# Kernel tuning notes

Measured on AMD Instinct MI355X. Metric: run time of the kernel, lower is better.

## Reference

```python
import jax, jax.numpy as jnp
import numpy as np

D_MODEL = 1024


def setup_inputs() -> dict:
    key = jax.random.key(0)
    ks = jax.random.split(key, 9)
    d = D_MODEL
    s = 1.0 / np.sqrt(d)
    return {
        "x": jax.random.normal(ks[0], (4, 2048, d), dtype=jnp.float32),
        "w_q": jax.random.normal(ks[1], (d, d), dtype=jnp.float32) * s,
        "b_q": jnp.zeros((d,), dtype=jnp.float32),
        "w_k": jax.random.normal(ks[2], (d, d), dtype=jnp.float32) * s,
        "b_k": jnp.zeros((d,), dtype=jnp.float32),
        "w_v": jax.random.normal(ks[3], (d, d), dtype=jnp.float32) * s,
        "b_v": jnp.zeros((d,), dtype=jnp.float32),
        "w_out": jax.random.normal(ks[4], (d, d), dtype=jnp.float32) * s,
        "b_out": jnp.zeros((d,), dtype=jnp.float32),
    }


def reference(x, w_q, b_q, w_k, b_k, w_v, b_v, w_out, b_out):
    d_model = x.shape[-1]
    # torch Linear: y = x @ W^T + b
    Q = jnp.einsum("bsd,ed->bse", x, w_q) + b_q
    K = jnp.einsum("bsd,ed->bse", x, w_k) + b_k
    V = jnp.einsum("bsd,ed->bse", x, w_v) + b_v
    scores = jnp.einsum("bqd,bkd->bqk", Q, K) / jnp.sqrt(jnp.float32(d_model)).astype(x.dtype)
    attn = jax.nn.softmax(scores, axis=-1)
    out = jnp.einsum("bqk,bkd->bqd", attn, V)
    return jnp.einsum("bsd,ed->bse", out, w_out) + b_out
```

## Files before the change

### kernel.cpp

```cpp
#include <hip/hip_runtime.h>


typedef __bf16 bf16x8 __attribute__((ext_vector_type(8)));
typedef float f32x4 __attribute__((ext_vector_type(4)));
typedef unsigned short ushort8 __attribute__((ext_vector_type(8)));

__device__ __forceinline__ unsigned short f32_to_bf16(float f) {
  unsigned int u = __float_as_uint(f);
  u += 0x7fffu + ((u >> 16) & 1u);
  return (unsigned short)(u >> 16);
}

__device__ __forceinline__ float bf16_to_f32(unsigned short u) {
  return __uint_as_float((unsigned int)u << 16);
}

__device__ __forceinline__ void load_lds16(const void* g, void* l) {
  __builtin_amdgcn_global_load_lds(
      (const __attribute__((address_space(1))) void*)g,
      (__attribute__((address_space(3))) void*)l, 16, 0, 0);
}

__global__ __launch_bounds__(256) void cast_f32_bf16(
    const float4* __restrict__ in, ushort4* __restrict__ out, int n4) {
  int i = blockIdx.x * 256 + threadIdx.x;
  if (i < n4) {
    float4 f = in[i];
    ushort4 u;
    u.x = f32_to_bf16(f.x);
    u.y = f32_to_bf16(f.y);
    u.z = f32_to_bf16(f.z);
    u.w = f32_to_bf16(f.w);
    out[i] = u;
  }
}

__global__ __launch_bounds__(256) void cast_weights(
    const float4* __restrict__ wq, const float4* __restrict__ wk,
    const float4* __restrict__ wv, const float4* __restrict__ wo,
    ushort4* __restrict__ wqkb, ushort4* __restrict__ wvb,
    ushort4* __restrict__ wob) {
  const int b = blockIdx.x;
  const int seg = b >> 10;
  const int idx = ((b & 1023) << 8) + threadIdx.x;
  const float4* src = seg == 0 ? wq : seg == 1 ? wk : seg == 2 ? wv : wo;
  ushort4* dst = seg == 0 ? wqkb
               : seg == 1 ? (wqkb + 262144)
               : seg == 2 ? wvb : wob;
  float4 f = src[idx];
  ushort4 u;
  u.x = f32_to_bf16(f.x);
  u.y = f32_to_bf16(f.y);
  u.z = f32_to_bf16(f.z);
  u.w = f32_to_bf16(f.w);
  dst[idx] = u;
}

__global__ __launch_bounds__(256) void concat_bias(
    const float* __restrict__ bq, const float* __restrict__ bk,
    float* __restrict__ bqk) {
  int i = blockIdx.x * 256 + threadIdx.x;
  bqk[i] = (i < 1024) ? bq[i] : bk[i - 1024];
}

__global__ __launch_bounds__(256) void gemm_bt(
    const unsigned short* __restrict__ A, const unsigned short* __restrict__ B,
    void* __restrict__ C, const float* __restrict__ bias,
    int M, int N, int K, int ldA, int ldB, int ldC,
    float alpha, int out_bf16, int bias_mode,
    long long sA, long long sB, long long sC) {
  __shared__ unsigned short As[128 * 64];
  __shared__ unsigned short Bs[128 * 64];

  const int bz = blockIdx.z;
  A += (long long)bz * sA;
  B += (long long)bz * sB;

  const int bm = blockIdx.y, bn = blockIdx.x;
  const int tid = threadIdx.x;
  const int lane = tid & 63, wave = tid >> 6;
  const int wr = wave >> 1, wc = wave & 1;
  const int l16 = lane & 15, quad = lane >> 4;

  f32x4 acc[4][4] = {};

  const int srow = tid >> 3;
  const int xr = srow & 7;
  const int scol = ((tid & 7) ^ xr) * 8;
  const unsigned short* gA = A + (long long)(bm * 128 + srow) * ldA + scol;
  const unsigned short* gB = B + (long long)(bn * 128 + srow) * ldB + scol;
  char* ldsA = (char*)As + wave * 1024;
  char* ldsB = (char*)Bs + wave * 1024;

  for (int k0 = 0; k0 < K; k0 += 64) {
#pragma unroll
    for (int r = 0; r < 4; r++)
      load_lds16(gA + k0 + (long long)r * 32 * ldA, ldsA + r * 4096);
#pragma unroll
    for (int r = 0; r < 4; r++)
      load_lds16(gB + k0 + (long long)r * 32 * ldB, ldsB + r * 4096);
    __syncthreads();

    const int swz = l16 & 7;
#pragma unroll
    for (int kk = 0; kk < 64; kk += 32) {
      bf16x8 af[4], bf[4];
      const int lc = (kk >> 3) + quad;
      const int pco = (lc ^ swz) * 8;
#pragma unroll
      for (int mi = 0; mi < 4; mi++)
        af[mi] = *(const bf16x8*)(As + (wr * 64 + mi * 16 + l16) * 64 + pco);
#pragma unroll
      for (int ni = 0; ni < 4; ni++)
        bf[ni] = *(const bf16x8*)(Bs + (wc * 64 + ni * 16 + l16) * 64 + pco);
#pragma unroll
      for (int mi = 0; mi < 4; mi++)
#pragma unroll
        for (int ni = 0; ni < 4; ni++)
          acc[mi][ni] = __builtin_amdgcn_mfma_f32_16x16x32_bf16(
              af[mi], bf[ni], acc[mi][ni], 0, 0, 0);
    }
    __syncthreads();
  }

  const int orow0 = bm * 128 + wr * 64 + quad * 4;
  const int ocol0 = bn * 128 + wc * 64 + l16;
  if (out_bf16) {
    unsigned short* Cp = (unsigned short*)C + (long long)bz * sC;
#pragma unroll
    for (int mi = 0; mi < 4; mi++)
#pragma unroll
      for (int ni = 0; ni < 4; ni++) {
        const int col = ocol0 + ni * 16;
        const float cb = (bias_mode == 1) ? bias[col] : 0.f;
#pragma unroll
        for (int r = 0; r < 4; r++) {
          const int row = orow0 + mi * 16 + r;
          const float bv = (bias_mode == 2) ? bias[row] : cb;
          const float o = acc[mi][ni][r] * alpha + bv;
          Cp[(long long)row * ldC + col] = f32_to_bf16(o);
        }
      }
  } else {
    float* Cp = (float*)C + (long long)bz * sC;
#pragma unroll
    for (int mi = 0; mi < 4; mi++)
#pragma unroll
      for (int ni = 0; ni < 4; ni++) {
        const int col = ocol0 + ni * 16;
        const float cb = (bias_mode == 1) ? bias[col] : 0.f;
#pragma unroll
        for (int r = 0; r < 4; r++) {
          const int row = orow0 + mi * 16 + r;
          const float bv = (bias_mode == 2) ? bias[row] : cb;
          const float o = acc[mi][ni][r] * alpha + bv;
          Cp[(long long)row * ldC + col] = o;
        }
      }
  }
}

__global__ __launch_bounds__(256) void softmax_rows_bf16(
    unsigned short* __restrict__ S) {
  const long long row = blockIdx.x;
  unsigned short* s = S + row * 2048;
  const int t = threadIdx.x;
  ushort8 u = *(const ushort8*)(s + t * 8);
  float v[8];
  float mx = -3.4e38f;
#pragma unroll
  for (int i = 0; i < 8; i++) {
    v[i] = bf16_to_f32(u[i]);
    mx = fmaxf(mx, v[i]);
  }
#pragma unroll
  for (int o = 32; o >= 1; o >>= 1) mx = fmaxf(mx, __shfl_xor(mx, o));
  __shared__ float red[4], red2[4];
  if ((t & 63) == 0) red[t >> 6] = mx;
  __syncthreads();
  mx = fmaxf(fmaxf(red[0], red[1]), fmaxf(red[2], red[3]));
  float sum = 0.f;
#pragma unroll
  for (int i = 0; i < 8; i++) {
    v[i] = __expf(v[i] - mx);
    sum += v[i];
  }
#pragma unroll
  for (int o = 32; o >= 1; o >>= 1) sum += __shfl_xor(sum, o);
  if ((t & 63) == 0) red2[t >> 6] = sum;
  __syncthreads();
  sum = red2[0] + red2[1] + red2[2] + red2[3];
  const float inv = 1.0f / sum;
  ushort8 w;
#pragma unroll
  for (int i = 0; i < 8; i++) w[i] = f32_to_bf16(v[i] * inv);
  *(ushort8*)(s + t * 8) = w;
}

extern "C" void kernel_launch(void* const* d_in, const int* in_sizes, int n_in,
                              void* d_out, int out_size, void* d_ws,
                              size_t ws_size, hipStream_t stream) {
  const float* x = (const float*)d_in[0];
  const float* wq = (const float*)d_in[1];
  const float* bq = (const float*)d_in[2];
  const float* wk = (const float*)d_in[3];
  const float* bk = (const float*)d_in[4];
  const float* wv = (const float*)d_in[5];
  const float* bv = (const float*)d_in[6];
  const float* wo = (const float*)d_in[7];
  const float* bo = (const float*)d_in[8];
  float* out = (float*)d_out;
  char* ws = (char*)d_ws;
  const size_t MB = 1ull << 20;

  unsigned short* xb   = (unsigned short*)(ws + 0);
  unsigned short* wqkb = (unsigned short*)(ws + 16 * MB);
  unsigned short* wvb  = (unsigned short*)(ws + 20 * MB);
  unsigned short* wob  = (unsigned short*)(ws + 22 * MB);
  unsigned short* QK   = (unsigned short*)(ws + 24 * MB);
  unsigned short* VT   = (unsigned short*)(ws + 56 * MB);
  unsigned short* S    = (unsigned short*)(ws + 72 * MB);
  float*          bqk  = (float*)(ws + 104 * MB);
  unsigned short* O    = xb;

  cast_f32_bf16<<<dim3(8192), dim3(256), 0, stream>>>((const float4*)x,
                                                      (ushort4*)xb, 2097152);
  cast_weights<<<dim3(4096), dim3(256), 0, stream>>>(
      (const float4*)wq, (const float4*)wk, (const float4*)wv,
      (const float4*)wo, (ushort4*)wqkb, (ushort4*)wvb, (ushort4*)wob);
  concat_bias<<<dim3(8), dim3(256), 0, stream>>>(bq, bk, bqk);

  gemm_bt<<<dim3(16, 64, 1), dim3(256), 0, stream>>>(
      xb, wqkb, QK, bqk, 8192, 2048, 1024, 1024, 1024, 2048, 1.f, 1, 1, 0, 0,
      0);

  gemm_bt<<<dim3(16, 8, 4), dim3(256), 0, stream>>>(
      wvb, xb, VT, bv, 1024, 2048, 1024, 1024, 1024, 2048, 1.f, 1, 2, 0,
      2048ll * 1024, 1024ll * 2048);

  gemm_bt<<<dim3(16, 16, 4), dim3(256), 0, stream>>>(
      QK, QK + 1024, S, nullptr, 2048, 2048, 1024, 2048, 2048, 2048, 0.03125f,
      1, 0, 2048ll * 2048, 2048ll * 2048, 2048ll * 2048);

  softmax_rows_bf16<<<dim3(8192), dim3(256), 0, stream>>>(S);

  gemm_bt<<<dim3(8, 16, 4), dim3(256), 0, stream>>>(
      S, VT, O, nullptr, 2048, 1024, 2048, 2048, 2048, 1024, 1.f, 1, 0,
      2048ll * 2048, 1024ll * 2048, 2048ll * 1024);

  gemm_bt<<<dim3(8, 64, 1), dim3(256), 0, stream>>>(
      O, wob, out, bo, 8192, 1024, 1024, 1024, 1024, 1024, 1.f, 0, 1, 0, 0, 0);
}
```

Measured before the change: 351.1 us.

## Split Q/K, V^T and P buffers into separate halves with 1024-wide row strides

The GEMM kernel gains dual A/B source pointers selected by a K-segment boundary and dual output pointers selected by a column split. With these, Q and K go to separate buffers, V^T is produced in two sequence halves, and softmax writes the probabilities into two half-width buffers. Every operand then has a leading dimension of 1024 rather than 2048. The likely aim is to cut strided 4KB row access patterns that cause channel or cache conflicts, at the cost of extra per-iteration branching and one more kernel launch for V.

```diff
diff --git a/kernel.cpp b/kernel.cpp
--- a/kernel.cpp
+++ b/kernel.cpp
@@ -64,18 +64,18 @@
 }
 
 __global__ __launch_bounds__(256) void gemm_bt(
-    const unsigned short* __restrict__ A, const unsigned short* __restrict__ B,
-    void* __restrict__ C, const float* __restrict__ bias,
-    int M, int N, int K, int ldA, int ldB, int ldC,
+    const unsigned short* __restrict__ A, const unsigned short* __restrict__ A2,
+    const unsigned short* __restrict__ B, const unsigned short* __restrict__ B2,
+    void* __restrict__ C, void* __restrict__ C2,
+    const float* __restrict__ bias,
+    int M, int N, int K, int Kseg, int Nsplit,
+    int ldA, int ldB, int ldC,
     float alpha, int out_bf16, int bias_mode,
     long long sA, long long sB, long long sC) {
   __shared__ unsigned short As[128 * 64];
   __shared__ unsigned short Bs[128 * 64];
 
   const int bz = blockIdx.z;
-  A += (long long)bz * sA;
-  B += (long long)bz * sB;
-
   const int bm = blockIdx.y, bn = blockIdx.x;
   const int tid = threadIdx.x;
   const int lane = tid & 63, wave = tid >> 6;
@@ -87,18 +87,27 @@
   const int srow = tid >> 3;
   const int xr = srow & 7;
   const int scol = ((tid & 7) ^ xr) * 8;
-  const unsigned short* gA = A + (long long)(bm * 128 + srow) * ldA + scol;
-  const unsigned short* gB = B + (long long)(bn * 128 + srow) * ldB + scol;
+  const long long aoff = (long long)bz * sA + (long long)(bm * 128 + srow) * ldA + scol;
+  const long long boff = (long long)bz * sB + (long long)(bn * 128 + srow) * ldB + scol;
+  const unsigned short* gA = A + aoff;
+  const unsigned short* gA2 = A2 + aoff;
+  const unsigned short* gB = B + boff;
+  const unsigned short* gB2 = B2 + boff;
   char* ldsA = (char*)As + wave * 1024;
   char* ldsB = (char*)Bs + wave * 1024;
 
   for (int k0 = 0; k0 < K; k0 += 64) {
+    const unsigned short* Ab;
+    const unsigned short* Bb;
+    int ko;
+    if (k0 < Kseg) { Ab = gA; Bb = gB; ko = k0; }
+    else           { Ab = gA2; Bb = gB2; ko = k0 - Kseg; }
 #pragma unroll
     for (int r = 0; r < 4; r++)
-      load_lds16(gA + k0 + (long long)r * 32 * ldA, ldsA + r * 4096);
+      load_lds16(Ab + ko + (long long)r * 32 * ldA, ldsA + r * 4096);
 #pragma unroll
     for (int r = 0; r < 4; r++)
-      load_lds16(gB + k0 + (long long)r * 32 * ldB, ldsB + r * 4096);
+      load_lds16(Bb + ko + (long long)r * 32 * ldB, ldsB + r * 4096);
     __syncthreads();
 
     const int swz = l16 & 7;
@@ -127,43 +136,50 @@
   const int ocol0 = bn * 128 + wc * 64 + l16;
   if (out_bf16) {
     unsigned short* Cp = (unsigned short*)C + (long long)bz * sC;
+    unsigned short* C2p = (unsigned short*)C2 + (long long)bz * sC;
 #pragma unroll
     for (int mi = 0; mi < 4; mi++)
 #pragma unroll
       for (int ni = 0; ni < 4; ni++) {
         const int col = ocol0 + ni * 16;
+        unsigned short* dst = (col < Nsplit) ? Cp : C2p;
+        const int cc = (col < Nsplit) ? col : col - Nsplit;
         const float cb = (bias_mode == 1) ? bias[col] : 0.f;
 #pragma unroll
         for (int r = 0; r < 4; r++) {
           const int row = orow0 + mi * 16 + r;
           const float bv = (bias_mode == 2) ? bias[row] : cb;
           const float o = acc[mi][ni][r] * alpha + bv;
-          Cp[(long long)row * ldC + col] = f32_to_bf16(o);
+          dst[(long long)row * ldC + cc] = f32_to_bf16(o);
         }
       }
   } else {
     float* Cp = (float*)C + (long long)bz * sC;
+    float* C2p = (float*)C2 + (long long)bz * sC;
 #pragma unroll
     for (int mi = 0; mi < 4; mi++)
 #pragma unroll
       for (int ni = 0; ni < 4; ni++) {
         const int col = ocol0 + ni * 16;
+        float* dst = (col < Nsplit) ? Cp : C2p;
+        const int cc = (col < Nsplit) ? col : col - Nsplit;
         const float cb = (bias_mode == 1) ? bias[col] : 0.f;
 #pragma unroll
         for (int r = 0; r < 4; r++) {
           const int row = orow0 + mi * 16 + r;
           const float bv = (bias_mode == 2) ? bias[row] : cb;
           const float o = acc[mi][ni][r] * alpha + bv;
-          Cp[(long long)row * ldC + col] = o;
+          dst[(long long)row * ldC + cc] = o;
         }
       }
   }
 }
 
-__global__ __launch_bounds__(256) void softmax_rows_bf16(
-    unsigned short* __restrict__ S) {
+__global__ __launch_bounds__(256) void softmax_split(
+    const unsigned short* __restrict__ S, unsigned short* __restrict__ P0,
+    unsigned short* __restrict__ P1) {
   const long long row = blockIdx.x;
-  unsigned short* s = S + row * 2048;
+  const unsigned short* s = S + row * 2048;
   const int t = threadIdx.x;
   ushort8 u = *(const ushort8*)(s + t * 8);
   float v[8];
@@ -194,7 +210,9 @@
   ushort8 w;
 #pragma unroll
   for (int i = 0; i < 8; i++) w[i] = f32_to_bf16(v[i] * inv);
-  *(ushort8*)(s + t * 8) = w;
+  unsigned short* dst =
+      (t < 128) ? (P0 + row * 1024 + t * 8) : (P1 + row * 1024 + (t - 128) * 8);
+  *(ushort8*)dst = w;
 }
 
 extern "C" void kernel_launch(void* const* d_in, const int* in_sizes, int n_in,
@@ -217,11 +235,13 @@
   unsigned short* wqkb = (unsigned short*)(ws + 16 * MB);
   unsigned short* wvb  = (unsigned short*)(ws + 20 * MB);
   unsigned short* wob  = (unsigned short*)(ws + 22 * MB);
-  unsigned short* QK   = (unsigned short*)(ws + 24 * MB);
-  unsigned short* VT   = (unsigned short*)(ws + 56 * MB);
+  unsigned short* Q    = (unsigned short*)(ws + 24 * MB);
+  unsigned short* Kb   = (unsigned short*)(ws + 40 * MB);
+  unsigned short* VT0  = (unsigned short*)(ws + 56 * MB);
+  unsigned short* VT1  = (unsigned short*)(ws + 64 * MB);
   unsigned short* S    = (unsigned short*)(ws + 72 * MB);
   float*          bqk  = (float*)(ws + 104 * MB);
-  unsigned short* O    = xb;
+  unsigned short* P0 = Q, *P1 = Kb, *O = xb;
 
   cast_f32_bf16<<<dim3(8192), dim3(256), 0, stream>>>((const float4*)x,
                                                       (ushort4*)xb, 2097152);
@@ -231,23 +251,28 @@
   concat_bias<<<dim3(8), dim3(256), 0, stream>>>(bq, bk, bqk);
 
   gemm_bt<<<dim3(16, 64, 1), dim3(256), 0, stream>>>(
-      xb, wqkb, QK, bqk, 8192, 2048, 1024, 1024, 1024, 2048, 1.f, 1, 1, 0, 0,
-      0);
-
-  gemm_bt<<<dim3(16, 8, 4), dim3(256), 0, stream>>>(
-      wvb, xb, VT, bv, 1024, 2048, 1024, 1024, 1024, 2048, 1.f, 1, 2, 0,
-      2048ll * 1024, 1024ll * 2048);
+      xb, xb, wqkb, wqkb, Q, Kb, bqk, 8192, 2048, 1024, 1024, 1024, 1024, 1024,
+      1024, 1.f, 1, 1, 0, 0, 0);
+
+  gemm_bt<<<dim3(8, 8, 4), dim3(256), 0, stream>>>(
+      wvb, wvb, xb, xb, VT0, VT0, bv, 1024, 1024, 1024, 1024, 1024, 1024, 1024,
+      1024, 1.f, 1, 2, 0, 2048ll * 1024, 1024ll * 1024);
+  gemm_bt<<<dim3(8, 8, 4), dim3(256), 0, stream>>>(
+      wvb, wvb, xb + 1024 * 1024, xb + 1024 * 1024, VT1, VT1, bv, 1024, 1024,
+      1024, 1024, 1024, 1024, 1024, 1024, 1.f, 1, 2, 0, 2048ll * 1024,
+      1024ll * 1024);
 
   gemm_bt<<<dim3(16, 16, 4), dim3(256), 0, stream>>>(
-      QK, QK + 1024, S, nullptr, 2048, 2048, 1024, 2048, 2048, 2048, 0.03125f,
-      1, 0, 2048ll * 2048, 2048ll * 2048, 2048ll * 2048);
-
-  softmax_rows_bf16<<<dim3(8192), dim3(256), 0, stream>>>(S);
+      Q, Q, Kb, Kb, S, S, nullptr, 2048, 2048, 1024, 1024, 2048, 1024, 1024,
+      2048, 0.03125f, 1, 0, 2048ll * 1024, 2048ll * 1024, 2048ll * 2048);
+
+  softmax_split<<<dim3(8192), dim3(256), 0, stream>>>(S, P0, P1);
 
   gemm_bt<<<dim3(8, 16, 4), dim3(256), 0, stream>>>(
-      S, VT, O, nullptr, 2048, 1024, 2048, 2048, 2048, 1024, 1.f, 1, 0,
-      2048ll * 2048, 1024ll * 2048, 2048ll * 1024);
+      P0, P1, VT0, VT1, O, O, nullptr, 2048, 1024, 2048, 1024, 1024, 1024,
+      1024, 1024, 1.f, 1, 0, 2048ll * 1024, 1024ll * 1024, 2048ll * 1024);
 
   gemm_bt<<<dim3(8, 64, 1), dim3(256), 0, stream>>>(
-      O, wob, out, bo, 8192, 1024, 1024, 1024, 1024, 1024, 1.f, 0, 1, 0, 0, 0);
-}
+      O, O, wob, wob, out, out, bo, 8192, 1024, 1024, 1024, 1024, 1024, 1024,
+      1024, 1.f, 0, 1, 0, 0, 0);
+}
```

New measurement: 382.4 us. 8.9% more time.
